# Kernel tuning notes

Measured on AMD Instinct MI355X. Metric: run time of the kernel, lower is better.

The kernel has to match this reference:

```python
import jax, jax.numpy as jnp
import numpy as np

B, T, D, KP1, R = 32, 1024, 64, 33, 8


def setup_inputs() -> dict:
    key = jax.random.key(0)
    k1, k2, k3, k4, k5, k6, k7, k8 = jax.random.split(key, 8)
    mu_t = jax.random.normal(k1, (B, T, D), dtype=jnp.float32)
    diag_var_t = jax.random.uniform(k2, (B, T, D), dtype=jnp.float32)  # nonneg variances
    F_t = 0.1 * jax.random.normal(k3, (B, T, D, R), dtype=jnp.float32)
    mu_k = jax.random.normal(k4, (KP1, D), dtype=jnp.float32)
    # SPD scale matrices Psi_k = A A^T / D + I  (cholesky-safe)
    A = jax.random.normal(k5, (KP1, D, D), dtype=jnp.float32)
    Psi = jnp.einsum('kde,kfe->kdf', A, A) / D + jnp.eye(D, dtype=jnp.float32)
    # nu_k > D + 1 so digamma((nu+1-i)/2) args are positive
    nu = D + 2.0 + 5.0 * jax.random.uniform(k6, (KP1,), dtype=jnp.float32)
    kappa = 0.5 + jax.random.uniform(k7, (KP1,), dtype=jnp.float32)
    mask = jax.random.randint(k8, (B, T), 0, 2) > 0
    return {"mu_t": mu_t, "diag_var_t": diag_var_t, "F_t": F_t,
            "mu_k": mu_k, "Psi": Psi, "nu": nu, "kappa": kappa, "mask": mask}


def _emission_loglik(mu_t, diag_var_t, F_t, mu_k, Psi, nu, kappa, mask):
    Kp1, Dd = mu_k.shape
    dt = mu_t.dtype
    # --- emission cache (chol_inv_logdet + expected Wishart stats) ---
    L = jnp.linalg.cholesky(Psi)                                   # [K,D,D]
    logdet_Psi = 2.0 * jnp.sum(jnp.log(jnp.diagonal(L, axis1=-2, axis2=-1)), axis=-1)
    eye = jnp.eye(Dd, dtype=dt)
    Psi_inv = jax.vmap(lambda Lk: jax.scipy.linalg.cho_solve((Lk, True), eye))(L)
    E_Lam = nu[:, None, None] * Psi_inv                            # [K,D,D]
    i = jnp.arange(1, Dd + 1, dtype=dt)[None, :]                   # [1,D]
    E_logdet = jnp.sum(jax.scipy.special.digamma((nu[:, None] + 1.0 - i) / 2.0), axis=1)
    E_logdet = E_logdet + Dd * jnp.log(jnp.asarray(2.0, dt)) - logdet_Psi
    const = 0.5 * (E_logdet - Dd * jnp.log(jnp.asarray(2.0 * np.pi, dt)))  # [K]
    # --- quadratic form + trace terms ---
    diff = mu_t[:, :, None, :] - mu_k[None, None, :, :]            # [B,T,K,D]
    quad_mean = jnp.einsum('btkd,kde,btke->btk', diff, E_Lam, diff)
    E_Lam_diag = jnp.diagonal(E_Lam, axis1=1, axis2=2)             # [K,D]
    tr_diag = jnp.einsum('kd,btd->btk', E_Lam_diag, diag_var_t)
    tr_lr = jnp.einsum('btdr,kde,bter->btk', F_t, E_Lam, F_t)
    D_over_kappa = (Dd / kappa)[None, None, :]
    logB = const[None, None, :] - 0.5 * (quad_mean + tr_diag + tr_lr + D_over_kappa)
    # masked steps are 'no observation' -> logB = 0
    logB = jnp.where(mask[:, :, None], logB, jnp.zeros_like(logB))
    return logB


def reference(mu_t, diag_var_t, F_t, mu_k, Psi, nu, kappa, mask):
    return _emission_loglik(mu_t, diag_var_t, F_t, mu_k, Psi, nu, kappa, mask)
```

## Files before the change

kernel.cpp:

```cpp
#include <hip/hip_runtime.h>


#define BT_TOTAL 32768
#define BT_BLK 16
#define NCHUNK 76

typedef _Float16 f16;
typedef __attribute__((ext_vector_type(8))) _Float16 f16x8;
typedef __attribute__((ext_vector_type(4))) _Float16 f16x4;
typedef __attribute__((ext_vector_type(2))) _Float16 h2;
typedef __attribute__((ext_vector_type(4))) float f32x4;
typedef struct { h2 p[4]; } h2q;

#if __has_builtin(__builtin_amdgcn_fdot2)
#define DOT2(a, b, c) __builtin_amdgcn_fdot2((a), (b), (c), false)
#else
#define DOT2(a, b, c) fmaf((float)(a)[0], (float)(b)[0], fmaf((float)(a)[1], (float)(b)[1], (c)))
#endif

__constant__ unsigned char PB_BJ[37] =
  {0, 1,1, 2,2,2, 3,3,3,3, 4,4,4,4,4, 5,5,5,5,5,5, 6,6,6,6,6,6,6, 7,7,7,7,7,7,7,7, 7};
__constant__ unsigned char PB_BI[37] =
  {0, 0,1, 0,1,2, 0,1,2,3, 0,1,2,3,4, 0,1,2,3,4,5, 0,1,2,3,4,5,6, 0,1,2,3,4,5,6,7, 7};

__device__ __forceinline__ float digammaf_(float x){
  float r = 0.f;
  while (x < 6.f){ r -= 1.f / x; x += 1.f; }
  float xi = 1.f / x;
  float xi2 = xi * xi;
  return r + logf(x) - 0.5f * xi
         - xi2 * (0.083333333333f - xi2 * (0.0083333333333f - xi2 * 0.0039682539683f));
}

__device__ __forceinline__ float wsum64(float x){
  #pragma unroll
  for (int o = 32; o > 0; o >>= 1) x += __shfl_down(x, o);
  return x;
}

__global__ __launch_bounds__(256) void prep_kernel(
    const float* __restrict__ mu_k, const float* __restrict__ Psi,
    const float* __restrict__ nu_a, const float* __restrict__ kap_a,
    const unsigned char* __restrict__ maskb,
    f16* __restrict__ BG, float* __restrict__ c0o,
    int* __restrict__ nactp, int* __restrict__ idxb)
{
  const int tid = threadIdx.x;

  if (blockIdx.x == 33){
    __shared__ int cnts[256];
    const int l = tid & 63;
    const bool byteMask =
        __any((maskb[4 * l + 1] | maskb[4 * l + 2] | maskb[4 * l + 3]) != 0);
    unsigned int nz[32];
    int cnt = 0;
    if (byteMask){
      const uint4* mv = (const uint4*)(maskb + (size_t)tid * 128);
      #pragma unroll
      for (int j = 0; j < 8; ++j){
        uint4 v = mv[j];
        unsigned int w0 = v.x, w1 = v.y, w2 = v.z, w3 = v.w;
        unsigned int b0 = ((w0 & 0xFFu) != 0) | (((w0 & 0xFF00u) != 0) << 1)
                        | (((w0 & 0xFF0000u) != 0) << 2) | (((w0 & 0xFF000000u) != 0) << 3);
        unsigned int b1 = ((w1 & 0xFFu) != 0) | (((w1 & 0xFF00u) != 0) << 1)
                        | (((w1 & 0xFF0000u) != 0) << 2) | (((w1 & 0xFF000000u) != 0) << 3);
        unsigned int b2 = ((w2 & 0xFFu) != 0) | (((w2 & 0xFF00u) != 0) << 1)
                        | (((w2 & 0xFF0000u) != 0) << 2) | (((w2 & 0xFF000000u) != 0) << 3);
        unsigned int b3 = ((w3 & 0xFFu) != 0) | (((w3 & 0xFF00u) != 0) << 1)
                        | (((w3 & 0xFF0000u) != 0) << 2) | (((w3 & 0xFF000000u) != 0) << 3);
        nz[4 * j + 0] = b0; nz[4 * j + 1] = b1; nz[4 * j + 2] = b2; nz[4 * j + 3] = b3;
        cnt += __popc(b0) + __popc(b1) + __popc(b2) + __popc(b3);
      }
    } else {
      const uint4* mv = (const uint4*)maskb + (size_t)tid * 32;
      #pragma unroll
      for (int j = 0; j < 32; ++j){
        uint4 v = mv[j];
        unsigned int b = (v.x != 0) | ((v.y != 0) << 1)
                       | ((v.z != 0) << 2) | ((v.w != 0) << 3);
        nz[j] = b;
        cnt += __popc(b);
      }
    }
    cnts[tid] = cnt;
    __syncthreads();
    for (int off = 1; off < 256; off <<= 1){
      int v = cnts[tid];
      int u = (tid >= off) ? cnts[tid - off] : 0;
      __syncthreads();
      cnts[tid] = v + u;
      __syncthreads();
    }
    const int nact = cnts[255];
    const int base = tid * 128;
    int wofsA = cnts[tid] - cnt;
    int wofsI = nact + base - wofsA;
    #pragma unroll
    for (int j = 0; j < 32; ++j){
      unsigned int b = nz[j];
      #pragma unroll
      for (int s = 0; s < 4; ++s){
        const int bt = base + 4 * j + s;
        if (b & (1u << s)) idxb[wofsA++] = bt;
        else               idxb[wofsI++] = bt;
      }
    }
    if (tid == 255) *nactp = nact;
    return;
  }

  const int k = blockIdx.x;
  const int row = tid & 63;
  const int ch  = tid >> 6;
  const int c0  = ch << 5;

  __shared__ float pr[2][128];
  __shared__ float fc[2][64];
  __shared__ float diag[64];
  __shared__ float muk[64];
  __shared__ float vpart[2][64];
  __shared__ float Ediag[64];

  float Wr[32];
  if (ch < 2){
    const float* Pg = Psi + (size_t)k * 4096 + (size_t)row * 64 + c0;
    #pragma unroll
    for (int c = 0; c < 32; ++c) Wr[c] = Pg[c];
  } else {
    #pragma unroll
    for (int c = 0; c < 32; ++c) Wr[c] = ((c0 - 64 + c) == row) ? 1.f : 0.f;
  }
  if (tid < 64) muk[tid] = mu_k[k * 64 + tid];
  if (row == 0){
    #pragma unroll
    for (int c = 0; c < 32; ++c) pr[0][c0 + c] = Wr[c];
  }
  if (ch == 0) fc[0][row] = Wr[0];
  __syncthreads();

  for (int jh = 0; jh < 2; ++jh){
    #pragma unroll
    for (int jl = 0; jl < 32; ++jl){
      const int j = jh * 32 + jl;
      const int cur = j & 1, nxt = cur ^ 1;
      float piv = pr[cur][j];
      float f = fc[cur][row] * __builtin_amdgcn_rcpf(piv);
      if (row == j && ch == 0) diag[j] = piv;
      if (row != j){
        #pragma unroll
        for (int c = 0; c < 32; ++c) Wr[c] = fmaf(-f, pr[cur][c0 + c], Wr[c]);
      }
      if (j < 63){
        if (row == j + 1){
          #pragma unroll
          for (int c = 0; c < 32; ++c) pr[nxt][c0 + c] = Wr[c];
        }
        if (jl < 31){ if (ch == jh)     fc[nxt][row] = Wr[jl + 1]; }
        else        { if (ch == jh + 1) fc[nxt][row] = Wr[0]; }
      }
      __syncthreads();
    }
  }

  const float nu = nu_a[k];
  const int j_k = k >> 4, kck = k & 15;

  if (ch >= 2){
    const int h = ch - 2;
    const float dinv = nu / diag[row];
    float vp = 0.f;
    #pragma unroll
    for (int c = 0; c < 32; ++c) vp = fmaf(Wr[c], muk[h * 32 + c], vp);
    vpart[h][row] = vp * dinv;
    const int d = row;
    const int bI = d >> 3;
    const int pch = (d >> 2) & 1;
    const int sHi = d & 3;
    #pragma unroll
    for (int cc = 0; cc < 32; ++cc){
      const int e = h * 32 + cc;
      const int bJ = e >> 3;
      float val = Wr[cc] * dinv;
      if (e == d) Ediag[row] = val;
      if (bI <= bJ){
        const int pb = ((bJ * (bJ + 1)) >> 1) + bI;
        const int ci = pb * 2 + pch;
        const float sc = (bI < bJ) ? 2.f : 1.f;
        BG[(size_t)((ci * 3 + j_k) * 64 + kck * 4 + sHi) * 8 + (e & 7)] = (f16)(val * sc);
      }
    }
  }
  __syncthreads();

  if (tid < 64){
    const int t = tid;
    float v = vpart[0][t] + vpart[1][t];
    const int g = (t >> 3) & 3, q = t & 7;
    const int cA = 72 + (t >> 5);
    const int cB = 74 + (t >> 5);
    BG[(size_t)((cA * 3 + j_k) * 64 + kck * 4 + g) * 8 + q] = (f16)(-2.f * v);
    BG[(size_t)((cB * 3 + j_k) * 64 + kck * 4 + g) * 8 + q] = (f16)(Ediag[t]);
    float c2 = wsum64(v * muk[t]);
    float dg = wsum64(digammaf_((nu - (float)t) * 0.5f));
    float ld = wsum64(logf(diag[t]));
    if (t == 0){
      const float LN2   = 0.69314718055994531f;
      const float LN2PI = 1.83787706640934548f;
      float Elogdet = dg + 64.f * LN2 - ld;
      float cst = 0.5f * (Elogdet - 64.f * LN2PI);
      c0o[k] = cst - 0.5f * c2 - 32.f / kap_a[k];
    }
  }
}

#define BUILD(AF, FD, MUD)                                                 \
  {                                                                        \
    float s_[8];                                                           \
    _Pragma("unroll")                                                      \
    for (int q_ = 0; q_ < 8; ++q_) s_[q_] = (MUD) * mue[q_];               \
    _Pragma("unroll")                                                      \
    for (int r_ = 0; r_ < 4; ++r_){                                        \
      h2 fp_ = { (FD)[2 * r_], (FD)[2 * r_ + 1] };                         \
      _Pragma("unroll")                                                    \
      for (int q_ = 0; q_ < 8; ++q_){                                      \
        h2 ep_ = { FeT[q_][2 * r_], FeT[q_][2 * r_ + 1] };                 \
        s_[q_] = DOT2(fp_, ep_, s_[q_]);                                   \
      }                                                                    \
    }                                                                      \
    _Pragma("unroll")                                                      \
    for (int q_ = 0; q_ < 8; ++q_) (AF)[q_] = (f16)s_[q_];                 \
  }

#define MFMA2(AF, B0, B1)                                                  \
  acc0 = __builtin_amdgcn_mfma_f32_16x16x32_f16((AF), (B0), acc0, 0, 0, 0);\
  acc1 = __builtin_amdgcn_mfma_f32_16x16x32_f16((AF), (B1), acc1, 0, 0, 0);

#define K32DOT(AF, B32)                                                    \
  {                                                                        \
    h2q afq_ = __builtin_bit_cast(h2q, (AF));                              \
    h2q bq_  = __builtin_bit_cast(h2q, (B32));                             \
    _Pragma("unroll")                                                      \
    for (int r_ = 0; r_ < 4; ++r_)                                         \
      acc32 = DOT2(afq_.p[r_], bq_.p[r_], acc32);                          \
  }

__global__ __launch_bounds__(128) void main_kernel(
    const float* __restrict__ mu_t, const float* __restrict__ var_t,
    const float* __restrict__ F_t,
    const f16* __restrict__ BG, const float* __restrict__ c0o,
    const int* __restrict__ nactp, const int* __restrict__ idxb,
    float* __restrict__ out)
{
  __shared__ __align__(16) f16 sG[BT_BLK][64][8];
  __shared__ __align__(16) f16 sMu[BT_BLK][64];
  __shared__ int sIdx[BT_BLK];

  const int tid = threadIdx.x;
  const int l = tid & 63;
  const int xh = tid >> 6;
  const int g = l >> 4;
  const int kc = l & 15;
  const int btl = kc;
  const int btSw = btl & 7;

  const int nact = *nactp;
  const int t0 = blockIdx.x * BT_BLK;
  const int nLoc = min(BT_BLK, max(0, nact - t0));

  if (tid < BT_BLK) sIdx[tid] = idxb[t0 + tid];
  __syncthreads();

  for (int i = tid; i < (BT_BLK - nLoc) * 33; i += 128){
    const int r = nLoc + i / 33;
    out[(size_t)sIdx[r] * 33 + (i % 33)] = 0.f;
  }
  if (nLoc == 0) return;

  {
    #pragma unroll
    for (int ii = 0; ii < 16; ++ii){
      int i = tid + ii * 128;
      int bt = i >> 7, rem = i & 127, d = rem >> 1, rb = (rem & 1) << 2;
      const float4* fg = (const float4*)(F_t + (size_t)sIdx[bt] * 512);
      float4 f = fg[rem];
      int dsw = d ^ (bt & 7);
      f16x4 ff = { (f16)f.x, (f16)f.y, (f16)f.z, (f16)f.w };
      *(f16x4*)&sG[bt][dsw][rb] = ff;
    }
    #pragma unroll
    for (int ii = 0; ii < 2; ++ii){
      int i = tid + ii * 128;
      int bt = i >> 4, e4 = i & 15, d0 = e4 << 2;
      const float4* mg = (const float4*)(mu_t + (size_t)sIdx[bt] * 64);
      float4 m4 = mg[e4];
      int dsw = (((d0 >> 3) ^ (bt & 7)) << 3) | (d0 & 7);
      f16x4 mm = { (f16)m4.x, (f16)m4.y, (f16)m4.z, (f16)m4.w };
      *(f16x4*)&sMu[bt][dsw] = mm;
    }
  }
  __syncthreads();

  const int ppStart = xh ? 19 : 0;
  const int ppEnd   = xh ? 36 : 19;

  f32x4 acc0 = {0.f,0.f,0.f,0.f}, acc1 = {0.f,0.f,0.f,0.f};
  float acc32 = 0.f;

  f16x8 FeT[8];
  float mue[8];

  const f16* bp   = BG + (size_t)(ppStart * 2) * 1536 + (size_t)(kc * 4 + g) * 8;
  const f16* bp32 = BG + (size_t)(ppStart * 2) * 1536 + 1024 + (size_t)g * 8;

  const int bI0 = PB_BI[ppStart];
  f16x8 fdA = *(const f16x8*)&sG[btl][(bI0 * 8 + g) ^ btSw][0];
  f16x8 fdB = *(const f16x8*)&sG[btl][(bI0 * 8 + 4 + g) ^ btSw][0];
  float mudA = (float)sMu[btl][((bI0 ^ btSw) << 3) | g];
  float mudB = (float)sMu[btl][((bI0 ^ btSw) << 3) | (4 + g)];

  f16x8 a0 = *(const f16x8*)(bp);
  f16x8 a1 = *(const f16x8*)(bp + 512);
  f16x8 b0v = *(const f16x8*)(bp + 1536);
  f16x8 b1v = *(const f16x8*)(bp + 1536 + 512);
  f16x8 w0v = *(const f16x8*)(bp32);
  f16x8 w1v = *(const f16x8*)(bp32 + 1536);
  bp += 3072;
  bp32 += 3072;

  int curBJ = -1;
  for (int pp = ppStart; pp < ppEnd; ++pp){
    const int bJ = PB_BJ[pp];
    if (bJ != curBJ){
      curBJ = bJ;
      #pragma unroll
      for (int q = 0; q < 8; ++q)
        FeT[q] = *(const f16x8*)&sG[btl][((bJ << 3) + q) ^ btSw][0];
      f16x8 mr = *(const f16x8*)&sMu[btl][((bJ ^ btSw) << 3)];
      #pragma unroll
      for (int q = 0; q < 8; ++q) mue[q] = (float)mr[q];
    }
    const int bIn = PB_BI[pp + 1];
    {
      f16x8 af;
      BUILD(af, fdA, mudA);
      MFMA2(af, a0, a1);
      K32DOT(af, w0v);
      a0 = *(const f16x8*)(bp);
      a1 = *(const f16x8*)(bp + 512);
      w0v = *(const f16x8*)(bp32);
      fdA = *(const f16x8*)&sG[btl][(bIn * 8 + g) ^ btSw][0];
      mudA = (float)sMu[btl][((bIn ^ btSw) << 3) | g];
    }
    {
      f16x8 af;
      BUILD(af, fdB, mudB);
      MFMA2(af, b0v, b1v);
      K32DOT(af, w1v);
      b0v = *(const f16x8*)(bp + 1536);
      b1v = *(const f16x8*)(bp + 1536 + 512);
      w1v = *(const f16x8*)(bp32 + 1536);
      fdB = *(const f16x8*)&sG[btl][(bIn * 8 + 4 + g) ^ btSw][0];
      mudB = (float)sMu[btl][((bIn ^ btSw) << 3) | (4 + g)];
    }
    bp += 3072;
    bp32 += 3072;
  }

  if (xh == 1){
    const f16* bpe   = BG + (size_t)72 * 1536 + (size_t)(kc * 4 + g) * 8;
    const f16* bpe32 = BG + (size_t)72 * 1536 + 1024 + (size_t)g * 8;
    #pragma unroll
    for (int m = 0; m < 4; ++m){
      f16x8 af;
      if (m < 2){
        af = *(const f16x8*)&sMu[btl][(((m * 4 + g) ^ btSw) << 3)];
      } else {
        const float* vr = var_t + (size_t)sIdx[btl] * 64 + (m - 2) * 32 + g * 8;
        f32x4 va = *(const f32x4*)(vr);
        f32x4 vb = *(const f32x4*)(vr + 4);
        #pragma unroll
        for (int r = 0; r < 4; ++r){ af[r] = (f16)va[r]; af[4 + r] = (f16)vb[r]; }
      }
      f16x8 e0 = *(const f16x8*)(bpe);
      f16x8 e1 = *(const f16x8*)(bpe + 512);
      f16x8 e32 = *(const f16x8*)(bpe32);
      MFMA2(af, e0, e1);
      K32DOT(af, e32);
      bpe += 1536;
      bpe32 += 1536;
    }
  }

  __syncthreads();
  float* sRedF = (float*)sG;
  if (xh == 1){
    const int bofs = l * 9;
    #pragma unroll
    for (int r = 0; r < 4; ++r){
      sRedF[bofs + r]     = acc0[r];
      sRedF[bofs + 4 + r] = acc1[r];
    }
    sRedF[bofs + 8] = acc32;
  }
  __syncthreads();
  if (xh == 0){
    const int bofs = l * 9;
    #pragma unroll
    for (int r = 0; r < 4; ++r){
      acc0[r] += sRedF[bofs + r];
      acc1[r] += sRedF[bofs + 4 + r];
    }
    acc32 += sRedF[bofs + 8];
    acc32 += __shfl_xor(acc32, 16);
    acc32 += __shfl_xor(acc32, 32);

    float c0a = c0o[kc];
    float c0b = c0o[16 + kc];
    float c0c = c0o[32];
    #pragma unroll
    for (int reg = 0; reg < 4; ++reg){
      int r16 = g * 4 + reg;
      if (r16 < nLoc){
        float* op = out + (size_t)sIdx[r16] * 33;
        op[kc]      = fmaf(-0.5f, acc0[reg], c0a);
        op[16 + kc] = fmaf(-0.5f, acc1[reg], c0b);
      }
    }
    if (g == 0 && kc < nLoc){
      out[(size_t)sIdx[kc] * 33 + 32] = fmaf(-0.5f, acc32, c0c);
    }
  }
}

extern "C" void kernel_launch(void* const* d_in, const int* in_sizes, int n_in,
                              void* d_out, int out_size, void* d_ws, size_t ws_size,
                              hipStream_t stream)
{
  const float* mu_t  = (const float*)d_in[0];
  const float* var_t = (const float*)d_in[1];
  const float* F_t   = (const float*)d_in[2];
  const float* mu_k  = (const float*)d_in[3];
  const float* Psi   = (const float*)d_in[4];
  const float* nu    = (const float*)d_in[5];
  const float* kap   = (const float*)d_in[6];
  const unsigned char* mask = (const unsigned char*)d_in[7];

  f16*   BG   = (f16*)d_ws;
  float* c0o  = (float*)((char*)d_ws + 233472);
  int*   nact = (int*)((char*)d_ws + 233472 + 256);
  int*   idxb = nact + 1;
  float* outp = (float*)d_out;

  hipLaunchKernelGGL(prep_kernel, dim3(34), dim3(256), 0, stream,
                     mu_k, Psi, nu, kap, mask, BG, c0o, nact, idxb);
  hipLaunchKernelGGL(main_kernel, dim3(BT_TOTAL / BT_BLK), dim3(128), 0, stream,
                     mu_t, var_t, F_t, BG, c0o, nact, idxb, outp);
}
```

Baseline: 66.84 us.

## Block the Gauss-Jordan elimination two pivots per step to halve barriers

The in-register Gauss-Jordan inversion of each Psi_k now eliminates two pivot rows per iteration instead of one. It computes the second pivot and combined coefficients analytically and applies both row updates in one fused pass, so the loop runs 32 iterations with 32 __syncthreads instead of 64. Separate double-buffered shared arrays hold the two pivot rows and pivot columns. The cost is extra scalar arithmetic per step, extra shared memory, and a slightly different rounding order in the inverse.

```diff
diff --git a/kernel.cpp b/kernel.cpp
--- a/kernel.cpp
+++ b/kernel.cpp
@@ -114,8 +114,10 @@
   const int ch  = tid >> 6;
   const int c0  = ch << 5;
 
-  __shared__ float pr[2][128];
-  __shared__ float fc[2][64];
+  __shared__ float prA[2][128];
+  __shared__ float prB[2][128];
+  __shared__ float fcA[2][64];
+  __shared__ float fcB[2][64];
   __shared__ float diag[64];
   __shared__ float muk[64];
   __shared__ float vpart[2][64];
@@ -133,30 +135,50 @@
   if (tid < 64) muk[tid] = mu_k[k * 64 + tid];
   if (row == 0){
     #pragma unroll
-    for (int c = 0; c < 32; ++c) pr[0][c0 + c] = Wr[c];
-  }
-  if (ch == 0) fc[0][row] = Wr[0];
-  __syncthreads();
-
+    for (int c = 0; c < 32; ++c) prA[0][c0 + c] = Wr[c];
+  }
+  if (row == 1){
+    #pragma unroll
+    for (int c = 0; c < 32; ++c) prB[0][c0 + c] = Wr[c];
+  }
+  if (ch == 0){ fcA[0][row] = Wr[0]; fcB[0][row] = Wr[1]; }
+  __syncthreads();
+
+  #pragma unroll
   for (int jh = 0; jh < 2; ++jh){
     #pragma unroll
-    for (int jl = 0; jl < 32; ++jl){
-      const int j = jh * 32 + jl;
-      const int cur = j & 1, nxt = cur ^ 1;
-      float piv = pr[cur][j];
-      float f = fc[cur][row] * __builtin_amdgcn_rcpf(piv);
-      if (row == j && ch == 0) diag[j] = piv;
-      if (row != j){
-        #pragma unroll
-        for (int c = 0; c < 32; ++c) Wr[c] = fmaf(-f, pr[cur][c0 + c], Wr[c]);
-      }
-      if (j < 63){
-        if (row == j + 1){
+    for (int ml = 0; ml < 16; ++ml){
+      const int m = jh * 16 + ml;
+      const int j = 2 * m;
+      const int cur = m & 1, nxt = cur ^ 1;
+      const float pivA = prA[cur][j];
+      const float rA1  = prA[cur][j + 1];
+      const float rcpA = __builtin_amdgcn_rcpf(pivA);
+      const float fJ1  = fcA[cur][j + 1] * rcpA;
+      const float pivB = fmaf(-fJ1, rA1, prB[cur][j + 1]);
+      const float rcpB = __builtin_amdgcn_rcpf(pivB);
+      const float f1 = (row == j) ? 0.f : fcA[cur][row] * rcpA;
+      const float v1 = (row == j) ? rA1 : fmaf(-f1, rA1, fcB[cur][row]);
+      const float f2 = (row == j + 1) ? 0.f : v1 * rcpB;
+      const float coefA = fmaf(-f2, fJ1, f1);
+      const float coefB = f2;
+      if (tid == 0){ diag[j] = pivA; diag[j + 1] = pivB; }
+      #pragma unroll
+      for (int c = 0; c < 32; ++c)
+        Wr[c] = fmaf(-coefA, prA[cur][c0 + c],
+                fmaf(-coefB, prB[cur][c0 + c], Wr[c]));
+      if (m < 31){
+        const int jn2 = j + 2, jn3 = j + 3;
+        if (row == jn2){
           #pragma unroll
-          for (int c = 0; c < 32; ++c) pr[nxt][c0 + c] = Wr[c];
+          for (int c = 0; c < 32; ++c) prA[nxt][c0 + c] = Wr[c];
         }
-        if (jl < 31){ if (ch == jh)     fc[nxt][row] = Wr[jl + 1]; }
-        else        { if (ch == jh + 1) fc[nxt][row] = Wr[0]; }
+        if (row == jn3){
+          #pragma unroll
+          for (int c = 0; c < 32; ++c) prB[nxt][c0 + c] = Wr[c];
+        }
+        if (ch == (jn2 >> 5)) fcA[nxt][row] = Wr[jn2 & 31];
+        if (ch == (jn3 >> 5)) fcB[nxt][row] = Wr[jn3 & 31];
       }
       __syncthreads();
     }
```

New measurement: 56.75 us. -15.1%, faster.
